# Kernel tuning notes

Hardware: AMD Instinct MI355X
Metric: run time of the kernel (lower is better)

Reference implementation:

```python
import jax, jax.numpy as jnp
import numpy as np

B, T, C, H = 16, 512, 256, 8
HS_T = C // H   # temporal head size = 32
HS_S = T // H   # spatial head size = 64
EPS = 1e-6


def _ln(x, w, b):
    m = x.mean(-1, keepdims=True)
    v = ((x - m) ** 2).mean(-1, keepdims=True)
    return (x - m) / jnp.sqrt(v + EPS) * w + b


def setup_inputs() -> dict:
    key = jax.random.key(0)
    ks = jax.random.split(key, 16)
    rn = lambda k, s, scale: jax.random.normal(k, s, dtype=jnp.float32) * scale
    inp = {
        "x_T": rn(ks[0], (B, T, C), 1.0),
        "x_S": rn(ks[1], (B, C, T), 1.0),
        # temporal attention: per-head q/k/v projections, stacked [H, hs, C]
        "Wq_t": rn(ks[2], (H, HS_T, C), C ** -0.5),
        "Wk_t": rn(ks[3], (H, HS_T, C), C ** -0.5),
        "Wv_t": rn(ks[4], (H, HS_T, C), C ** -0.5),
        "Wo": rn(ks[5], (C, C), C ** -0.5),
        # spatial attention: per-head q/k over the time axis, stacked [H, hs_s, T]
        "Wq_s": rn(ks[6], (H, HS_S, T), T ** -0.5),
        "Wk_s": rn(ks[7], (H, HS_S, T), T ** -0.5),
        # feed-forward blocks (expansion_factor=4)
        "ff1_w1": rn(ks[8], (4 * C, C), C ** -0.5),
        "ff1_b1": jnp.zeros((4 * C,), jnp.float32),
        "ff1_w2": rn(ks[9], (C, 4 * C), (4 * C) ** -0.5),
        "ff1_b2": jnp.zeros((C,), jnp.float32),
        "ff2_w1": rn(ks[10], (4 * C, C), C ** -0.5),
        "ff2_b1": jnp.zeros((4 * C,), jnp.float32),
        "ff2_w2": rn(ks[11], (C, 4 * C), (4 * C) ** -0.5),
        "ff2_b2": jnp.zeros((C,), jnp.float32),
        # layernorm affine params
        "t_ln1_w": jnp.ones((C,), jnp.float32), "t_ln1_b": jnp.zeros((C,), jnp.float32),
        "t_ln2_w": jnp.ones((C,), jnp.float32), "t_ln2_b": jnp.zeros((C,), jnp.float32),
        "s_ln1_w": jnp.ones((T,), jnp.float32), "s_ln1_b": jnp.zeros((T,), jnp.float32),
        "fus_ln_w": jnp.ones((C,), jnp.float32), "fus_ln_b": jnp.zeros((C,), jnp.float32),
    }
    return inp


def reference(x_T, x_S, Wq_t, Wk_t, Wv_t, Wo, Wq_s, Wk_s,
              ff1_w1, ff1_b1, ff1_w2, ff1_b2, ff2_w1, ff2_b1, ff2_w2, ff2_b2,
              t_ln1_w, t_ln1_b, t_ln2_w, t_ln2_b, s_ln1_w, s_ln1_b,
              fus_ln_w, fus_ln_b):
    # ---- temporal (causal) multi-head attention ----
    h = _ln(x_T, t_ln1_w, t_ln1_b)                         # [B,T,C]
    q = jnp.einsum('btc,hdc->bhtd', h, Wq_t)
    k = jnp.einsum('btc,hdc->bhtd', h, Wk_t)
    v = jnp.einsum('btc,hdc->bhtd', h, Wv_t)
    scores = jnp.einsum('bhtd,bhsd->bhts', q, k) / jnp.sqrt(jnp.float32(HS_T))
    causal = jnp.tril(jnp.ones((T, T), dtype=bool))
    scores = jnp.where(causal, scores, -jnp.inf)
    att = jax.nn.softmax(scores, axis=-1)
    o = jnp.einsum('bhts,bhsd->bhtd', att, v)              # [B,H,T,hs]
    o = o.transpose(0, 2, 1, 3).reshape(B, T, C)           # concat heads
    attn_out = o @ Wo.T
    x = x_T + attn_out
    # FFN 1
    h2 = _ln(x, t_ln2_w, t_ln2_b)
    f = jax.nn.relu(h2 @ ff1_w1.T + ff1_b1) @ ff1_w2.T + ff1_b2
    temporal_out = x + f                                   # [B,T,C]
    # ---- spatial (non-causal) attention over neurons ----
    hs = _ln(x_S, s_ln1_w, s_ln1_b)                        # [B,C,T]
    qs = jnp.einsum('bct,hdt->bhcd', hs, Wq_s)
    ks = jnp.einsum('bct,hdt->bhcd', hs, Wk_s)
    sc = jnp.einsum('bhcd,bhed->bhce', qs, ks) / jnp.sqrt(jnp.float32(HS_S))
    spatial_weights = jax.nn.softmax(sc, axis=-1).mean(axis=1)   # [B,C,C], mean over heads
    # ---- fusion ----
    fused = jnp.einsum('bce,bte->btc', spatial_weights, temporal_out)
    x2 = temporal_out + fused
    h3 = _ln(x2, fus_ln_w, fus_ln_b)
    f2 = jax.nn.relu(h3 @ ff2_w1.T + ff2_b1) @ ff2_w2.T + ff2_b2
    out = x2 + f2
    return out, spatial_weights
```

## Files before the change

### kernel.cpp

```cpp
#include <hip/hip_runtime.h>
#include <hip/hip_bf16.h>

typedef __hip_bfloat16 bf16;
typedef __attribute__((ext_vector_type(8))) short short8;
typedef __attribute__((ext_vector_type(4))) float f32x4;

#define F_BIAS 1
#define F_RELU 2
#define F_RES  4

__device__ __forceinline__ void st_out(float* p, float v){ *p = v; }
__device__ __forceinline__ void st_out(bf16* p, float v){ *p = __float2bfloat16(v); }
__device__ __forceinline__ short f2bs(float f){
  bf16 h = __float2bfloat16(f);
  return *reinterpret_cast<short*>(&h);
}

__device__ __forceinline__ void gl_lds16(const void* g, void* l){
  __builtin_amdgcn_global_load_lds(
      (const __attribute__((address_space(1))) void*)g,
      (__attribute__((address_space(3))) void*)l, 16, 0, 0);
}

struct ProArgs {
  const float* wsrc[10];
  bf16* wdst[10];
  const float *xT, *xS, *tl1w, *tl1b, *sl1w, *sl1b;
  bf16 *hT, *hS;
};

__device__ void ln_body(bf16* __restrict__ dst, const float* __restrict__ src,
                        const float* __restrict__ w, const float* __restrict__ bvec,
                        int row, int rowLen){
  int tid = threadIdx.x;
  const float* s = src + (size_t)row*rowLen;
  float x0 = s[tid];
  float x1 = (rowLen > 256) ? s[tid+256] : 0.0f;
  float sum = x0 + x1, sq = x0*x0 + x1*x1;
  #pragma unroll
  for (int off=32; off; off>>=1){
    sum += __shfl_down(sum, off, 64);
    sq  += __shfl_down(sq , off, 64);
  }
  __shared__ float sbs[4], sbq[4];
  int wid = tid>>6, lane = tid&63;
  if (lane==0){ sbs[wid]=sum; sbq[wid]=sq; }
  __syncthreads();
  if (tid==0){
    float a=0, b2=0;
    for (int i=0;i<4;i++){ a+=sbs[i]; b2+=sbq[i]; }
    sbs[0]=a; sbq[0]=b2;
  }
  __syncthreads();
  float inv  = 1.0f/(float)rowLen;
  float mean = sbs[0]*inv;
  float var  = sbq[0]*inv - mean*mean;
  float rstd = rsqrtf(var + 1e-6f);
  bf16* d = dst + (size_t)row*rowLen;
  d[tid] = __float2bfloat16((x0-mean)*rstd*w[tid] + bvec[tid]);
  if (rowLen > 256)
    d[tid+256] = __float2bfloat16((x1-mean)*rstd*w[tid+256] + bvec[tid+256]);
}

__global__ __launch_bounds__(256) void prologue(ProArgs a){
  int blk = blockIdx.x;
  if (blk < 1792){
    int v = blk*256 + threadIdx.x;
    int e = v*4;
    int seg = (e>=65536)+(e>=131072)+(e>=196608)+(e>=262144)+(e>=524288)
            + (e>=786432)+(e>=1048576)+(e>=1310720)+(e>=1572864);
    const int starts[10] = {0,65536,131072,196608,262144,524288,786432,
                            1048576,1310720,1572864};
    int off = e - starts[seg];
    float4 f = *(const float4*)(a.wsrc[seg] + off);
    short4 o;
    o.x = f2bs(f.x); o.y = f2bs(f.y); o.z = f2bs(f.z); o.w = f2bs(f.w);
    *(short4*)((short*)a.wdst[seg] + off) = o;
  } else if (blk < 1792 + 8192){
    ln_body(a.hT, a.xT, a.tl1w, a.tl1b, blk-1792, 256);
  } else {
    ln_body(a.hS, a.xS, a.sl1w, a.sl1b, blk-9984, 512);
  }
}

template<int BM, int BK>
__device__ __forceinline__ void gemm_body(
    const bf16* __restrict__ A, const bf16* __restrict__ B,
    float* __restrict__ outF, bf16* __restrict__ outB,
    const float* __restrict__ bias, const float* __restrict__ resid,
    int K, int lda, int ldb, int ldc, int flags, int m0, int n0){
  __shared__ short As[BM*BK];
  __shared__ short Bs[128*BK];
  int tid = threadIdx.x;
  int w = tid>>6, lane = tid&63, quad = lane>>4, l16 = lane&15;
  constexpr int WM = BM/2;
  constexpr int MF = WM/16;
  constexpr int CPR = BK/8;
  constexpr int CA = BM*CPR/256;
  constexpr int CB = 128*CPR/256;
  int wm = (w>>1)*WM, wn = (w&1)*64;
  f32x4 acc[MF][4];
  #pragma unroll
  for (int r=0;r<MF;r++)
    #pragma unroll
    for (int j=0;j<4;j++)
      acc[r][j] = (f32x4){0.f,0.f,0.f,0.f};

  for (int k0 = 0; k0 < K; k0 += BK){
    #pragma unroll
    for (int c=0;c<CA;c++){
      int ch = tid + c*256;
      int row = ch / CPR, p = ch % CPR;
      gl_lds16(A + (size_t)(m0+row)*lda + k0 + ((p ^ (row&(CPR-1)))*8),
               &As[row*BK + p*8]);
    }
    #pragma unroll
    for (int c=0;c<CB;c++){
      int ch = tid + c*256;
      int row = ch / CPR, p = ch % CPR;
      gl_lds16(B + (size_t)(n0+row)*ldb + k0 + ((p ^ (row&(CPR-1)))*8),
               &Bs[row*BK + p*8]);
    }
    __syncthreads();
    #pragma unroll
    for (int ks=0; ks<BK/32; ++ks){
      short8 af[MF], bfr[4];
      #pragma unroll
      for (int r=0;r<MF;r++){
        int rr = wm + r*16 + l16;
        af[r] = *(short8*)&As[rr*BK + (((ks*4+quad) ^ (rr&(CPR-1)))*8)];
      }
      #pragma unroll
      for (int j=0;j<4;j++){
        int rr = wn + j*16 + l16;
        bfr[j] = *(short8*)&Bs[rr*BK + (((ks*4+quad) ^ (rr&(CPR-1)))*8)];
      }
      #pragma unroll
      for (int r=0;r<MF;r++)
        #pragma unroll
        for (int j=0;j<4;j++)
          acc[r][j] = __builtin_amdgcn_mfma_f32_16x16x32_bf16(af[r], bfr[j], acc[r][j], 0,0,0);
    }
    __syncthreads();
  }
  #pragma unroll
  for (int r=0;r<MF;r++){
    int mb = m0 + wm + r*16 + quad*4;
    #pragma unroll
    for (int j=0;j<4;j++){
      int n = n0 + wn + j*16 + l16;
      float bv = (flags & F_BIAS) ? bias[n] : 0.0f;
      #pragma unroll
      for (int e=0;e<4;e++){
        float v = acc[r][j][e] + bv;
        if (flags & F_RELU) v = fmaxf(v, 0.0f);
        long long idx = (long long)(mb+e)*ldc + n;
        if (flags & F_RES) v += resid[idx];
        if (outF) outF[idx] = v;
        if (outB) st_out(outB + idx, v);
      }
    }
  }
}

template<int BM, int BK>
__global__ __launch_bounds__(256) void gemm_mfma(
    const bf16* __restrict__ A, const bf16* __restrict__ B,
    float* __restrict__ outF, bf16* __restrict__ outB,
    const float* __restrict__ bias, const float* __restrict__ resid,
    int K, int lda, int ldb, int ldc, int flags){
  gemm_body<BM,BK>(A,B,outF,outB,bias,resid,K,lda,ldb,ldc,flags,
                   blockIdx.x*BM, blockIdx.y*128);
}

struct GArgs {
  const bf16 *A, *B;
  float* outF; bf16* outB;
  const float *bias, *resid;
  int K, lda, ldb, ldc, flags, ty;
};
__global__ __launch_bounds__(256) void gemm_dual(GArgs g0, GArgs g1, int n0){
  int id = blockIdx.x;
  bool first = id < n0;
  const GArgs& g = first ? g0 : g1;
  int t = first ? id : id - n0;
  int bx = t / g.ty, by = t - bx*g.ty;
  gemm_body<128,64>(g.A, g.B, g.outF, g.outB, g.bias, g.resid,
                    g.K, g.lda, g.ldb, g.ldc, g.flags, bx*128, by*128);
}

__global__ __launch_bounds__(256) void gemm_ln(
    const bf16* __restrict__ A, const bf16* __restrict__ B,
    float* __restrict__ outF, bf16* __restrict__ outLN,
    const float* __restrict__ resid,
    const float* __restrict__ lnw, const float* __restrict__ lnb,
    int K, int lda, int ldb, int flags,
    long long sA, long long sB, long long sO, long long sR){
  int bz = blockIdx.z;
  A += (size_t)bz*sA;
  B += (size_t)bz*sB;
  long long obase = (long long)bz*sO;
  __shared__ short As[32*64];
  __shared__ short Bs[256*64];
  __shared__ float redS[2][32], redQ[2][32];
  int tid = threadIdx.x;
  int m0 = blockIdx.x*32;
  int w = tid>>6, lane = tid&63, quad = lane>>4, l16 = lane&15;
  int wm = (w>>1)*16, wn = (w&1)*128;
  f32x4 acc[8];
  #pragma unroll
  for (int j=0;j<8;j++) acc[j] = (f32x4){0.f,0.f,0.f,0.f};

  for (int k0 = 0; k0 < K; k0 += 64){
    {
      int row = tid >> 3, p = tid & 7;
      gl_lds16(A + (size_t)(m0+row)*lda + k0 + ((p ^ (row&7))*8),
               &As[row*64 + p*8]);
    }
    #pragma unroll
    for (int c=0;c<8;c++){
      int ch = tid + c*256;
      int row = ch >> 3, p = ch & 7;
      gl_lds16(B + (size_t)row*ldb + k0 + ((p ^ (row&7))*8),
               &Bs[row*64 + p*8]);
    }
    __syncthreads();
    #pragma unroll
    for (int ks=0; ks<2; ++ks){
      int rr = wm + l16;
      short8 af = *(short8*)&As[rr*64 + (((ks*4+quad) ^ (rr&7))*8)];
      #pragma unroll
      for (int j=0;j<8;j++){
        int rb = wn + j*16 + l16;
        short8 bfr = *(short8*)&Bs[rb*64 + (((ks*4+quad) ^ (rb&7))*8)];
        acc[j] = __builtin_amdgcn_mfma_f32_16x16x32_bf16(af, bfr, acc[j], 0,0,0);
      }
    }
    __syncthreads();
  }
  #pragma unroll
  for (int e=0;e<4;e++){
    int row = wm + quad*4 + e;
    float s = 0.f, q2 = 0.f;
    #pragma unroll
    for (int j=0;j<8;j++){
      float v = acc[j][e];
      if (flags & F_RES)
        v += resid[(long long)bz*sR + (long long)(m0+row)*256 + wn + j*16 + l16];
      acc[j][e] = v;
      s += v; q2 += v*v;
    }
    #pragma unroll
    for (int off=1; off<16; off<<=1){
      s  += __shfl_xor(s , off, 16);
      q2 += __shfl_xor(q2, off, 16);
    }
    if (l16==0){ redS[w&1][row] = s; redQ[w&1][row] = q2; }
  }
  __syncthreads();
  #pragma unroll
  for (int e=0;e<4;e++){
    int row = wm + quad*4 + e;
    float tot = redS[0][row] + redS[1][row];
    float tq  = redQ[0][row] + redQ[1][row];
    float mean = tot * (1.0f/256.0f);
    float var  = tq * (1.0f/256.0f) - mean*mean;
    float rstd = rsqrtf(var + 1e-6f);
    #pragma unroll
    for (int j=0;j<8;j++){
      int col = wn + j*16 + l16;
      float v = acc[j][e];
      long long idx = obase + (long long)(m0+row)*256 + col;
      if (outF) outF[idx] = v;
      outLN[idx] = __float2bfloat16((v-mean)*rstd*lnw[col] + lnb[col]);
    }
  }
}

__device__ __forceinline__ int fsw(int row){ return (row>>1)&3; }
__global__ __launch_bounds__(256) void flash_mfma(
    const bf16* __restrict__ qkv, bf16* __restrict__ o){
  int qt = (int)gridDim.x - 1 - (int)blockIdx.x;
  int h = blockIdx.y, b = blockIdx.z;
  int tid = threadIdx.x;
  int w = tid>>6, lane = tid&63, quad = lane>>4, l16 = lane&15;
  __shared__ bf16 Qs[64*32];
  __shared__ bf16 Ks[64*32];
  __shared__ bf16 Vt[32*72];
  __shared__ bf16 Ps[64*72];
  const bf16* base = qkv + (size_t)b*512*768;
  int t0 = qt*64;
  int srow = tid>>2, spos = tid&3;
  gl_lds16(base + (size_t)(t0+srow)*768 + h*32 + ((spos ^ fsw(srow))*8),
           &Qs[srow*32 + spos*8]);
  f32x4 accO[2];
  accO[0] = (f32x4){0.f,0.f,0.f,0.f};
  accO[1] = (f32x4){0.f,0.f,0.f,0.f};
  float m_i[4], l_i[4];
  #pragma unroll
  for (int e=0;e<4;e++){ m_i[e] = -3.0e38f; l_i[e] = 0.0f; }
  const float scale = 0.17677669529663687f;

  for (int kt = 0; kt <= qt; ++kt){
    int s0 = kt*64;
    __syncthreads();
    {
      const bf16* rp = base + (size_t)(s0+srow)*768 + h*32;
      gl_lds16(rp + 256 + ((spos ^ fsw(srow))*8), &Ks[srow*32 + spos*8]);
      short8 v = *(const short8*)(rp + 512 + spos*8);
      #pragma unroll
      for (int q=0;q<8;q++){
        short tmp = v[q];
        Vt[(spos*8+q)*72 + srow] = *(bf16*)&tmp;
      }
    }
    __syncthreads();
    int rq = w*16 + l16;
    short8 aq = *(short8*)&Qs[rq*32 + ((quad ^ fsw(rq))*8)];
    f32x4 S[4];
    #pragma unroll
    for (int j2=0;j2<4;j2++){
      int rk = j2*16 + l16;
      short8 bk = *(short8*)&Ks[rk*32 + ((quad ^ fsw(rk))*8)];
      S[j2] = __builtin_amdgcn_mfma_f32_16x16x32_bf16(aq, bk,
                (f32x4){0.f,0.f,0.f,0.f}, 0,0,0);
    }
    bool diag = (kt == qt);
    int qrow_base = t0 + w*16 + quad*4;
    #pragma unroll
    for (int e=0;e<4;e++){
      float sv[4];
      #pragma unroll
      for (int j2=0;j2<4;j2++){
        float x = S[j2][e]*scale;
        if (diag && (s0 + j2*16 + l16 > qrow_base + e)) x = -3.0e38f;
        sv[j2] = x;
      }
      float mx = fmaxf(fmaxf(sv[0],sv[1]), fmaxf(sv[2],sv[3]));
      #pragma unroll
      for (int off=1; off<16; off<<=1) mx = fmaxf(mx, __shfl_xor(mx, off, 64));
      float m_new = fmaxf(m_i[e], mx);
      float alpha = __expf(m_i[e]-m_new);
      float rs = 0.0f;
      #pragma unroll
      for (int j2=0;j2<4;j2++){
        float p = __expf(sv[j2]-m_new);
        rs += p;
        Ps[(w*16+quad*4+e)*72 + j2*16 + l16] = __float2bfloat16(p);
      }
      #pragma unroll
      for (int off=1; off<16; off<<=1) rs += __shfl_xor(rs, off, 64);
      l_i[e] = l_i[e]*alpha + rs;
      m_i[e] = m_new;
      accO[0][e] *= alpha;
      accO[1][e] *= alpha;
    }
    __syncthreads();
    #pragma unroll
    for (int sh=0; sh<2; ++sh){
      short8 ap = *(short8*)&Ps[(w*16+l16)*72 + sh*32 + quad*8];
      #pragma unroll
      for (int dh=0; dh<2; ++dh){
        short8 bv = *(short8*)&Vt[(dh*16+l16)*72 + sh*32 + quad*8];
        accO[dh] = __builtin_amdgcn_mfma_f32_16x16x32_bf16(ap, bv, accO[dh], 0,0,0);
      }
    }
  }
  #pragma unroll
  for (int e=0;e<4;e++){
    float inv = 1.0f/l_i[e];
    int t = t0 + w*16 + quad*4 + e;
    bf16* op = o + ((size_t)(b*512+t))*256 + h*32 + l16;
    op[0]  = __float2bfloat16(accO[0][e]*inv);
    op[16] = __float2bfloat16(accO[1][e]*inv);
  }
}

__device__ void spatial_body(const bf16* __restrict__ qk,
                             float* __restrict__ out1, bf16* __restrict__ swB,
                             int ct, int b){
  int tid = threadIdx.x;
  int w = tid>>6, lane = tid&63, quad = lane>>4, l16 = lane&15;
  __shared__ bf16 Qall[16*512];
  __shared__ bf16 Ks[256*64];
  __shared__ float redM[4][16], redS2[4][16];
  const bf16* qbase = qk + ((size_t)(b*256 + ct*16))*1024;
  #pragma unroll
  for (int c=0;c<4;c++){
    int ch = tid + c*256;
    int row = ch>>6, p = ch&63;
    gl_lds16(qbase + (size_t)row*1024 + ((p ^ (row&7))*8), &Qall[row*512 + p*8]);
  }
  float fRes[4][4];
  #pragma unroll
  for (int j=0;j<4;j++)
    #pragma unroll
    for (int e=0;e<4;e++) fRes[j][e] = 0.0f;

  for (int h=0; h<8; ++h){
    __syncthreads();
    #pragma unroll
    for (int c=0;c<8;c++){
      int ch = tid + c*256;
      int e = ch>>3, p = ch&7;
      gl_lds16(qk + ((size_t)(b*256 + e))*1024 + 512 + h*64 + ((p ^ (e&7))*8),
               &Ks[e*64 + p*8]);
    }
    __syncthreads();
    f32x4 acc[4];
    #pragma unroll
    for (int j=0;j<4;j++) acc[j] = (f32x4){0.f,0.f,0.f,0.f};
    #pragma unroll
    for (int ks=0; ks<2; ++ks){
      int g = h*8 + ks*4 + quad;
      short8 aq = *(short8*)&Qall[l16*512 + ((g ^ (l16&7))*8)];
      #pragma unroll
      for (int j=0;j<4;j++){
        int e = w*64 + j*16 + l16;
        short8 bk = *(short8*)&Ks[e*64 + (((ks*4+quad) ^ (e&7))*8)];
        acc[j] = __builtin_amdgcn_mfma_f32_16x16x32_bf16(aq, bk, acc[j], 0,0,0);
      }
    }
    #pragma unroll
    for (int e=0;e<4;e++){
      float m = -3.0e38f;
      #pragma unroll
      for (int j=0;j<4;j++){
        float s = acc[j][e]*0.125f;
        acc[j][e] = s;
        m = fmaxf(m, s);
      }
      #pragma unroll
      for (int off=1; off<16; off<<=1) m = fmaxf(m, __shfl_xor(m, off, 16));
      if (l16==0) redM[w][quad*4+e] = m;
    }
    __syncthreads();
    #pragma unroll
    for (int e=0;e<4;e++){
      int r = quad*4+e;
      float m = fmaxf(fmaxf(redM[0][r],redM[1][r]), fmaxf(redM[2][r],redM[3][r]));
      float s = 0.0f;
      #pragma unroll
      for (int j=0;j<4;j++){
        float p = __expf(acc[j][e]-m);
        acc[j][e] = p; s += p;
      }
      #pragma unroll
      for (int off=1; off<16; off<<=1) s += __shfl_xor(s, off, 16);
      if (l16==0) redS2[w][r] = s;
    }
    __syncthreads();
    #pragma unroll
    for (int e=0;e<4;e++){
      int r = quad*4+e;
      float tot = redS2[0][r]+redS2[1][r]+redS2[2][r]+redS2[3][r];
      float inv = 0.125f/tot;
      #pragma unroll
      for (int j=0;j<4;j++) fRes[j][e] += acc[j][e]*inv;
    }
  }
  #pragma unroll
  for (int e=0;e<4;e++){
    int c = ct*16 + quad*4 + e;
    size_t rb = ((size_t)b*256 + c)*256;
    #pragma unroll
    for (int j=0;j<4;j++){
      int col = w*64 + j*16 + l16;
      out1[rb+col] = fRes[j][e];
      swB[rb+col]  = __float2bfloat16(fRes[j][e]);
    }
  }
}

__global__ __launch_bounds__(256) void mixed_l2(
    const bf16* __restrict__ gA, const bf16* __restrict__ gB,
    float* __restrict__ gOutF, bf16* __restrict__ gOutB,
    const float* __restrict__ gBias, const float* __restrict__ gResid,
    const bf16* __restrict__ qk, float* __restrict__ out1,
    bf16* __restrict__ swB){
  int id = blockIdx.x;
  if (id < 256){
    int bx = id >> 1, by = id & 1;
    gemm_body<64,64>(gA, gB, gOutF, gOutB, gBias, gResid,
                     1024, 1024, 1024, 256, F_BIAS|F_RES, bx*64, by*128);
  } else {
    int t = id - 256;
    spatial_body(qk, out1, swB, t & 15, t >> 4);
  }
}

extern "C" void kernel_launch(void* const* d_in, const int* in_sizes, int n_in,
                              void* d_out, int out_size, void* d_ws, size_t ws_size,
                              hipStream_t stream){
  (void)in_sizes; (void)n_in; (void)out_size; (void)ws_size;
  const float* x_T  = (const float*)d_in[0];
  const float* x_S  = (const float*)d_in[1];
  const float* Wq_t = (const float*)d_in[2];
  const float* Wk_t = (const float*)d_in[3];
  const float* Wv_t = (const float*)d_in[4];
  const float* Wo   = (const float*)d_in[5];
  const float* Wq_s = (const float*)d_in[6];
  const float* Wk_s = (const float*)d_in[7];
  const float* f1w1 = (const float*)d_in[8];
  const float* f1b1 = (const float*)d_in[9];
  const float* f1w2 = (const float*)d_in[10];
  const float* f1b2 = (const float*)d_in[11];
  const float* f2w1 = (const float*)d_in[12];
  const float* f2b1 = (const float*)d_in[13];
  const float* f2w2 = (const float*)d_in[14];
  const float* f2b2 = (const float*)d_in[15];
  const float* tl1w = (const float*)d_in[16];
  const float* tl1b = (const float*)d_in[17];
  const float* tl2w = (const float*)d_in[18];
  const float* tl2b = (const float*)d_in[19];
  const float* sl1w = (const float*)d_in[20];
  const float* sl1b = (const float*)d_in[21];
  const float* flw  = (const float*)d_in[22];
  const float* flb  = (const float*)d_in[23];

  float* ws = (float*)d_ws;
  size_t off = 0;
  bf16*  Wqkvb  = (bf16*)(ws + off); off += 768*256/2;
  bf16*  Wob    = (bf16*)(ws + off); off += 256*256/2;
  bf16*  f1w1b  = (bf16*)(ws + off); off += 1024*256/2;
  bf16*  f1w2b  = (bf16*)(ws + off); off += 256*1024/2;
  bf16*  f2w1b  = (bf16*)(ws + off); off += 1024*256/2;
  bf16*  f2w2b  = (bf16*)(ws + off); off += 256*1024/2;
  bf16*  WSb    = (bf16*)(ws + off); off += 1024*512/2;
  bf16*  bufHb  = (bf16*)(ws + off); off += (size_t)8192*256/2;
  bf16*  bufHSb = (bf16*)(ws + off); off += (size_t)4096*512/2;
  bf16*  bufQKVb= (bf16*)(ws + off); off += (size_t)8192*768/2;
  bf16*  bufBigB= (bf16*)(ws + off); off += (size_t)8192*1024/2;
  bf16*  bufOb  = (bf16*)(ws + off); off += (size_t)8192*256/2;
  bf16*  bufTOb = (bf16*)(ws + off); off += (size_t)8192*256/2;
  bf16*  swB    = (bf16*)(ws + off); off += (size_t)16*256*256/2;
  bf16*  qkB    = (bf16*)(ws + off); off += (size_t)4096*1024/2;
  float* bufX   = ws + off; off += (size_t)8192*256;
  float* bufTO  = ws + off; off += (size_t)8192*256;
  float* bufX2  = ws + off; off += (size_t)8192*256;

  float* out0 = (float*)d_out;
  float* out1 = out0 + (size_t)16*512*256;

  ProArgs pa;
  pa.wsrc[0]=Wq_t;  pa.wdst[0]=Wqkvb;
  pa.wsrc[1]=Wk_t;  pa.wdst[1]=Wqkvb+65536;
  pa.wsrc[2]=Wv_t;  pa.wdst[2]=Wqkvb+131072;
  pa.wsrc[3]=Wo;    pa.wdst[3]=Wob;
  pa.wsrc[4]=f1w1;  pa.wdst[4]=f1w1b;
  pa.wsrc[5]=f1w2;  pa.wdst[5]=f1w2b;
  pa.wsrc[6]=f2w1;  pa.wdst[6]=f2w1b;
  pa.wsrc[7]=f2w2;  pa.wdst[7]=f2w2b;
  pa.wsrc[8]=Wq_s;  pa.wdst[8]=WSb;
  pa.wsrc[9]=Wk_s;  pa.wdst[9]=WSb+262144;
  pa.xT=x_T; pa.xS=x_S; pa.tl1w=tl1w; pa.tl1b=tl1b;
  pa.sl1w=sl1w; pa.sl1b=sl1b; pa.hT=bufHb; pa.hS=bufHSb;
  prologue<<<14080,256,0,stream>>>(pa);

  GArgs gq, gs;
  gq.A=bufHb;  gq.B=Wqkvb; gq.outF=nullptr; gq.outB=bufQKVb;
  gq.bias=nullptr; gq.resid=nullptr;
  gq.K=256; gq.lda=256; gq.ldb=256; gq.ldc=768; gq.flags=0; gq.ty=6;
  gs.A=bufHSb; gs.B=WSb;   gs.outF=nullptr; gs.outB=qkB;
  gs.bias=nullptr; gs.resid=nullptr;
  gs.K=512; gs.lda=512; gs.ldb=512; gs.ldc=1024; gs.flags=0; gs.ty=8;
  gemm_dual<<<640,256,0,stream>>>(gq, gs, 384);

  flash_mfma<<<dim3(8,8,16),256,0,stream>>>(bufQKVb, bufOb);
  gemm_ln<<<dim3(256,1,1),256,0,stream>>>(bufOb, Wob, bufX, bufHb,
        x_T, tl2w, tl2b, 256, 256,256, F_RES, 0,0,0,0);
  gemm_mfma<128,64><<<dim3(64,8),256,0,stream>>>(bufHb, f1w1b, nullptr, bufBigB,
        f1b1, nullptr, 256, 256,256,1024, F_BIAS|F_RELU);
  mixed_l2<<<512,256,0,stream>>>(bufBigB, f1w2b, bufTO, bufTOb, f1b2, bufX,
        qkB, out1, swB);
  gemm_ln<<<dim3(16,1,16),256,0,stream>>>(bufTOb, swB, bufX2, bufHb,
        bufTO, flw, flb, 256, 256,256, F_RES,
        131072, 65536, 131072, 131072);
  gemm_mfma<128,64><<<dim3(64,8),256,0,stream>>>(bufHb, f2w1b, nullptr, bufBigB,
        f2b1, nullptr, 256, 256,256,1024, F_BIAS|F_RELU);
  gemm_mfma<64,64><<<dim3(128,2),256,0,stream>>>(bufBigB, f2w2b, out0, nullptr,
        f2b2, bufX2, 1024, 1024,1024,256, F_BIAS|F_RES);
}
```

Before: 287.8 us.

## Load GEMM MFMA fragments directly from global memory instead of staging through LDS

Removes the LDS staging (global_load_lds plus swizzled shared-memory reads and two barriers per K step) from gemm_body and gemm_ln. Each wave now loads its A and B short8 fragments straight from global memory for every 32-wide K step, with a 2x unroll. This drops barrier and LDS traffic and frees shared memory for occupancy, but gives up reuse across waves: B tiles are fetched once per wave pair rather than once per block, and the per-lane 16-byte strided loads depend on L1/L2 hits and may coalesce poorly.

Measured after the change: 342.2 us. +18.9%, slower.

```diff
diff --git a/kernel.cpp b/kernel.cpp
--- a/kernel.cpp
+++ b/kernel.cpp
@@ -83,21 +83,16 @@
   }
 }
 
-template<int BM, int BK>
+template<int BM>
 __device__ __forceinline__ void gemm_body(
     const bf16* __restrict__ A, const bf16* __restrict__ B,
     float* __restrict__ outF, bf16* __restrict__ outB,
     const float* __restrict__ bias, const float* __restrict__ resid,
     int K, int lda, int ldb, int ldc, int flags, int m0, int n0){
-  __shared__ short As[BM*BK];
-  __shared__ short Bs[128*BK];
   int tid = threadIdx.x;
   int w = tid>>6, lane = tid&63, quad = lane>>4, l16 = lane&15;
   constexpr int WM = BM/2;
   constexpr int MF = WM/16;
-  constexpr int CPR = BK/8;
-  constexpr int CA = BM*CPR/256;
-  constexpr int CB = 128*CPR/256;
   int wm = (w>>1)*WM, wn = (w&1)*64;
   f32x4 acc[MF][4];
   #pragma unroll
@@ -106,42 +101,22 @@
     for (int j=0;j<4;j++)
       acc[r][j] = (f32x4){0.f,0.f,0.f,0.f};
 
-  for (int k0 = 0; k0 < K; k0 += BK){
-    #pragma unroll
-    for (int c=0;c<CA;c++){
-      int ch = tid + c*256;
-      int row = ch / CPR, p = ch % CPR;
-      gl_lds16(A + (size_t)(m0+row)*lda + k0 + ((p ^ (row&(CPR-1)))*8),
-               &As[row*BK + p*8]);
-    }
-    #pragma unroll
-    for (int c=0;c<CB;c++){
-      int ch = tid + c*256;
-      int row = ch / CPR, p = ch % CPR;
-      gl_lds16(B + (size_t)(n0+row)*ldb + k0 + ((p ^ (row&(CPR-1)))*8),
-               &Bs[row*BK + p*8]);
-    }
-    __syncthreads();
-    #pragma unroll
-    for (int ks=0; ks<BK/32; ++ks){
-      short8 af[MF], bfr[4];
-      #pragma unroll
-      for (int r=0;r<MF;r++){
-        int rr = wm + r*16 + l16;
-        af[r] = *(short8*)&As[rr*BK + (((ks*4+quad) ^ (rr&(CPR-1)))*8)];
-      }
-      #pragma unroll
-      for (int j=0;j<4;j++){
-        int rr = wn + j*16 + l16;
-        bfr[j] = *(short8*)&Bs[rr*BK + (((ks*4+quad) ^ (rr&(CPR-1)))*8)];
-      }
-      #pragma unroll
-      for (int r=0;r<MF;r++)
-        #pragma unroll
-        for (int j=0;j<4;j++)
-          acc[r][j] = __builtin_amdgcn_mfma_f32_16x16x32_bf16(af[r], bfr[j], acc[r][j], 0,0,0);
-    }
-    __syncthreads();
+  const bf16* Ab = A + (size_t)(m0+wm+l16)*lda + quad*8;
+  const bf16* Bb = B + (size_t)(n0+wn+l16)*ldb + quad*8;
+  #pragma unroll 2
+  for (int k0 = 0; k0 < K; k0 += 32){
+    short8 af[MF], bfr[4];
+    #pragma unroll
+    for (int r=0;r<MF;r++)
+      af[r] = *(const short8*)(Ab + (size_t)r*16*lda + k0);
+    #pragma unroll
+    for (int j=0;j<4;j++)
+      bfr[j] = *(const short8*)(Bb + (size_t)j*16*ldb + k0);
+    #pragma unroll
+    for (int r=0;r<MF;r++)
+      #pragma unroll
+      for (int j=0;j<4;j++)
+        acc[r][j] = __builtin_amdgcn_mfma_f32_16x16x32_bf16(af[r], bfr[j], acc[r][j], 0,0,0);
   }
   #pragma unroll
   for (int r=0;r<MF;r++){
@@ -163,14 +138,14 @@
   }
 }
 
-template<int BM, int BK>
+template<int BM>
 __global__ __launch_bounds__(256) void gemm_mfma(
     const bf16* __restrict__ A, const bf16* __restrict__ B,
     float* __restrict__ outF, bf16* __restrict__ outB,
     const float* __restrict__ bias, const float* __restrict__ resid,
     int K, int lda, int ldb, int ldc, int flags){
-  gemm_body<BM,BK>(A,B,outF,outB,bias,resid,K,lda,ldb,ldc,flags,
-                   blockIdx.x*BM, blockIdx.y*128);
+  gemm_body<BM>(A,B,outF,outB,bias,resid,K,lda,ldb,ldc,flags,
+                blockIdx.x*BM, blockIdx.y*128);
 }
 
 struct GArgs {
@@ -185,8 +160,8 @@
   const GArgs& g = first ? g0 : g1;
   int t = first ? id : id - n0;
   int bx = t / g.ty, by = t - bx*g.ty;
-  gemm_body<128,64>(g.A, g.B, g.outF, g.outB, g.bias, g.resid,
-                    g.K, g.lda, g.ldb, g.ldc, g.flags, bx*128, by*128);
+  gemm_body<128>(g.A, g.B, g.outF, g.outB, g.bias, g.resid,
+                 g.K, g.lda, g.ldb, g.ldc, g.flags, bx*128, by*128);
 }
 
 __global__ __launch_bounds__(256) void gemm_ln(
@@ -200,8 +175,6 @@
   A += (size_t)bz*sA;
   B += (size_t)bz*sB;
   long long obase = (long long)bz*sO;
-  __shared__ short As[32*64];
-  __shared__ short Bs[256*64];
   __shared__ float redS[2][32], redQ[2][32];
   int tid = threadIdx.x;
   int m0 = blockIdx.x*32;
@@ -211,32 +184,18 @@
   #pragma unroll
   for (int j=0;j<8;j++) acc[j] = (f32x4){0.f,0.f,0.f,0.f};
 
-  for (int k0 = 0; k0 < K; k0 += 64){
-    {
-      int row = tid >> 3, p = tid & 7;
-      gl_lds16(A + (size_t)(m0+row)*lda + k0 + ((p ^ (row&7))*8),
-               &As[row*64 + p*8]);
-    }
-    #pragma unroll
-    for (int c=0;c<8;c++){
-      int ch = tid + c*256;
-      int row = ch >> 3, p = ch & 7;
-      gl_lds16(B + (size_t)row*ldb + k0 + ((p ^ (row&7))*8),
-               &Bs[row*64 + p*8]);
-    }
-    __syncthreads();
-    #pragma unroll
-    for (int ks=0; ks<2; ++ks){
-      int rr = wm + l16;
-      short8 af = *(short8*)&As[rr*64 + (((ks*4+quad) ^ (rr&7))*8)];
-      #pragma unroll
-      for (int j=0;j<8;j++){
-        int rb = wn + j*16 + l16;
-        short8 bfr = *(short8*)&Bs[rb*64 + (((ks*4+quad) ^ (rb&7))*8)];
-        acc[j] = __builtin_amdgcn_mfma_f32_16x16x32_bf16(af, bfr, acc[j], 0,0,0);
-      }
-    }
-    __syncthreads();
+  const bf16* Ab = A + (size_t)(m0+wm+l16)*lda + quad*8;
+  const bf16* Bb = B + (size_t)(wn+l16)*ldb + quad*8;
+  #pragma unroll 2
+  for (int k0 = 0; k0 < K; k0 += 32){
+    short8 af = *(const short8*)(Ab + k0);
+    short8 bfr[8];
+    #pragma unroll
+    for (int j=0;j<8;j++)
+      bfr[j] = *(const short8*)(Bb + (size_t)j*16*ldb + k0);
+    #pragma unroll
+    for (int j=0;j<8;j++)
+      acc[j] = __builtin_amdgcn_mfma_f32_16x16x32_bf16(af, bfr[j], acc[j], 0,0,0);
   }
   #pragma unroll
   for (int e=0;e<4;e++){
@@ -481,8 +440,8 @@
   int id = blockIdx.x;
   if (id < 256){
     int bx = id >> 1, by = id & 1;
-    gemm_body<64,64>(gA, gB, gOutF, gOutB, gBias, gResid,
-                     1024, 1024, 1024, 256, F_BIAS|F_RES, bx*64, by*128);
+    gemm_body<64>(gA, gB, gOutF, gOutB, gBias, gResid,
+                  1024, 1024, 1024, 256, F_BIAS|F_RES, bx*64, by*128);
   } else {
     int t = id - 256;
     spatial_body(qk, out1, swB, t & 15, t >> 4);
@@ -569,15 +528,15 @@
   flash_mfma<<<dim3(8,8,16),256,0,stream>>>(bufQKVb, bufOb);
   gemm_ln<<<dim3(256,1,1),256,0,stream>>>(bufOb, Wob, bufX, bufHb,
         x_T, tl2w, tl2b, 256, 256,256, F_RES, 0,0,0,0);
-  gemm_mfma<128,64><<<dim3(64,8),256,0,stream>>>(bufHb, f1w1b, nullptr, bufBigB,
+  gemm_mfma<128><<<dim3(64,8),256,0,stream>>>(bufHb, f1w1b, nullptr, bufBigB,
         f1b1, nullptr, 256, 256,256,1024, F_BIAS|F_RELU);
   mixed_l2<<<512,256,0,stream>>>(bufBigB, f1w2b, bufTO, bufTOb, f1b2, bufX,
         qkB, out1, swB);
   gemm_ln<<<dim3(16,1,16),256,0,stream>>>(bufTOb, swB, bufX2, bufHb,
         bufTO, flw, flb, 256, 256,256, F_RES,
         131072, 65536, 131072, 131072);
-  gemm_mfma<128,64><<<dim3(64,8),256,0,stream>>>(bufHb, f2w1b, nullptr, bufBigB,
+  gemm_mfma<128><<<dim3(64,8),256,0,stream>>>(bufHb, f2w1b, nullptr, bufBigB,
         f2b1, nullptr, 256, 256,256,1024, F_BIAS|F_RELU);
-  gemm_mfma<64,64><<<dim3(128,2),256,0,stream>>>(bufBigB, f2w2b, out0, nullptr,
+  gemm_mfma<64><<<dim3(128,2),256,0,stream>>>(bufBigB, f2w2b, out0, nullptr,
         f2b2, bufX2, 1024, 1024,1024,256, F_BIAS|F_RES);
 }
```

## Co-schedule spatial attention with flash attention instead of FFN1 second GEMM

Applied to the files above, without the earlier changes.

Moves the spatial attention blocks out of the mixed kernel that shared a launch with the FFN1 down-projection GEMM and into a new combined kernel alongside causal flash attention. Both bodies share one shared-memory buffer carved by offsets, and the FFN1 down-projection now runs as a standalone GEMM launch. The aim is to fill the GPU better during flash attention, whose causal tiles are unevenly loaded, using the independent spatial work. The cost is a larger static shared-memory footprint of about 49KB for every flash block, which may lower flash occupancy compared with its original roughly 22KB.

New measurement: 300.2 us. +4.3%, slower.

```diff
diff --git a/kernel.cpp b/kernel.cpp
--- a/kernel.cpp
+++ b/kernel.cpp
@@ -278,16 +278,14 @@
 }
 
 __device__ __forceinline__ int fsw(int row){ return (row>>1)&3; }
-__global__ __launch_bounds__(256) void flash_mfma(
-    const bf16* __restrict__ qkv, bf16* __restrict__ o){
-  int qt = (int)gridDim.x - 1 - (int)blockIdx.x;
-  int h = blockIdx.y, b = blockIdx.z;
+__device__ void flash_body(const bf16* __restrict__ qkv, bf16* __restrict__ o,
+                           int qt, int h, int b, char* smem){
+  bf16* Qs = (bf16*)smem;
+  bf16* Ks = (bf16*)(smem + 4096);
+  bf16* Vt = (bf16*)(smem + 8192);
+  bf16* Ps = (bf16*)(smem + 12800);
   int tid = threadIdx.x;
   int w = tid>>6, lane = tid&63, quad = lane>>4, l16 = lane&15;
-  __shared__ bf16 Qs[64*32];
-  __shared__ bf16 Ks[64*32];
-  __shared__ bf16 Vt[32*72];
-  __shared__ bf16 Ps[64*72];
   const bf16* base = qkv + (size_t)b*512*768;
   int t0 = qt*64;
   int srow = tid>>2, spos = tid&3;
@@ -378,12 +376,13 @@
 
 __device__ void spatial_body(const bf16* __restrict__ qk,
                              float* __restrict__ out1, bf16* __restrict__ swB,
-                             int ct, int b){
+                             int ct, int b, char* smem){
+  bf16* Qall = (bf16*)smem;
+  bf16* Ks   = (bf16*)(smem + 16384);
+  float* redM  = (float*)(smem + 49152);
+  float* redS2 = (float*)(smem + 49408);
   int tid = threadIdx.x;
   int w = tid>>6, lane = tid&63, quad = lane>>4, l16 = lane&15;
-  __shared__ bf16 Qall[16*512];
-  __shared__ bf16 Ks[256*64];
-  __shared__ float redM[4][16], redS2[4][16];
   const bf16* qbase = qk + ((size_t)(b*256 + ct*16))*1024;
   #pragma unroll
   for (int c=0;c<4;c++){
@@ -432,13 +431,13 @@
       }
       #pragma unroll
       for (int off=1; off<16; off<<=1) m = fmaxf(m, __shfl_xor(m, off, 16));
-      if (l16==0) redM[w][quad*4+e] = m;
+      if (l16==0) redM[w*16 + quad*4+e] = m;
     }
     __syncthreads();
     #pragma unroll
     for (int e=0;e<4;e++){
       int r = quad*4+e;
-      float m = fmaxf(fmaxf(redM[0][r],redM[1][r]), fmaxf(redM[2][r],redM[3][r]));
+      float m = fmaxf(fmaxf(redM[r],redM[16+r]), fmaxf(redM[32+r],redM[48+r]));
       float s = 0.0f;
       #pragma unroll
       for (int j=0;j<4;j++){
@@ -447,13 +446,13 @@
       }
       #pragma unroll
       for (int off=1; off<16; off<<=1) s += __shfl_xor(s, off, 16);
-      if (l16==0) redS2[w][r] = s;
+      if (l16==0) redS2[w*16 + r] = s;
     }
     __syncthreads();
     #pragma unroll
     for (int e=0;e<4;e++){
       int r = quad*4+e;
-      float tot = redS2[0][r]+redS2[1][r]+redS2[2][r]+redS2[3][r];
+      float tot = redS2[r]+redS2[16+r]+redS2[32+r]+redS2[48+r];
       float inv = 0.125f/tot;
       #pragma unroll
       for (int j=0;j<4;j++) fRes[j][e] += acc[j][e]*inv;
@@ -472,20 +471,18 @@
   }
 }
 
-__global__ __launch_bounds__(256) void mixed_l2(
-    const bf16* __restrict__ gA, const bf16* __restrict__ gB,
-    float* __restrict__ gOutF, bf16* __restrict__ gOutB,
-    const float* __restrict__ gBias, const float* __restrict__ gResid,
+__global__ __launch_bounds__(256) void flash_spatial(
+    const bf16* __restrict__ qkv, bf16* __restrict__ o,
     const bf16* __restrict__ qk, float* __restrict__ out1,
     bf16* __restrict__ swB){
+  __shared__ __align__(16) char smem[49664];
   int id = blockIdx.x;
-  if (id < 256){
-    int bx = id >> 1, by = id & 1;
-    gemm_body<64,64>(gA, gB, gOutF, gOutB, gBias, gResid,
-                     1024, 1024, 1024, 256, F_BIAS|F_RES, bx*64, by*128);
+  if (id < 1024){
+    int b = id >> 6, h = (id >> 3) & 7, qt = 7 - (id & 7);
+    flash_body(qkv, o, qt, h, b, smem);
   } else {
-    int t = id - 256;
-    spatial_body(qk, out1, swB, t & 15, t >> 4);
+    int t = id - 1024;
+    spatial_body(qk, out1, swB, t & 15, t >> 4, smem);
   }
 }
 
@@ -566,13 +563,14 @@
   gs.K=512; gs.lda=512; gs.ldb=512; gs.ldc=1024; gs.flags=0; gs.ty=8;
   gemm_dual<<<640,256,0,stream>>>(gq, gs, 384);
 
-  flash_mfma<<<dim3(8,8,16),256,0,stream>>>(bufQKVb, bufOb);
+  flash_spatial<<<1280,256,0,stream>>>(bufQKVb, bufOb, qkB, out1, swB);
+
   gemm_ln<<<dim3(256,1,1),256,0,stream>>>(bufOb, Wob, bufX, bufHb,
         x_T, tl2w, tl2b, 256, 256,256, F_RES, 0,0,0,0);
   gemm_mfma<128,64><<<dim3(64,8),256,0,stream>>>(bufHb, f1w1b, nullptr, bufBigB,
         f1b1, nullptr, 256, 256,256,1024, F_BIAS|F_RELU);
-  mixed_l2<<<512,256,0,stream>>>(bufBigB, f1w2b, bufTO, bufTOb, f1b2, bufX,
-        qkB, out1, swB);
+  gemm_mfma<64,64><<<dim3(128,2),256,0,stream>>>(bufBigB, f1w2b, bufTO, bufTOb,
+        f1b2, bufX, 1024, 1024,1024,256, F_BIAS|F_RES);
   gemm_ln<<<dim3(16,1,16),256,0,stream>>>(bufTOb, swB, bufX2, bufHb,
         bufTO, flw, flb, 256, 256,256, F_RES,
         131072, 65536, 131072, 131072);
```
